# Optimization experiments

Hardware: AMD Instinct MI355X
Metric: run time of the kernel (lower is better)

## Reference

```python
import jax, jax.numpy as jnp
import numpy as np


def setup_inputs() -> dict:
    key = jax.random.key(0)
    k1, k2 = jax.random.split(key)
    B, N, M = 32, 4096, 4096
    pred = jax.random.normal(k1, (B, N, 3), dtype=jnp.float32)
    target = jax.random.normal(k2, (B, M, 3), dtype=jnp.float32)
    return {"pred": pred, "target": target}


def reference(pred, target):
    # pairwise euclidean distances: [B, N, M]
    # d2 = |p|^2 + |t|^2 - 2 p.t  (matches torch.cdist p=2)
    p2 = jnp.sum(pred * pred, axis=-1)                      # [B, N]
    t2 = jnp.sum(target * target, axis=-1)                  # [B, M]
    pt = jnp.einsum('bnd,bmd->bnm', pred, target)           # [B, N, M]
    d2 = p2[:, :, None] + t2[:, None, :] - 2.0 * pt
    dist = jnp.sqrt(jnp.maximum(d2, 0.0))                   # [B, N, M]
    min_d = jnp.min(dist, axis=2)                           # [B, N]
    return jnp.mean(min_d)
```

## Files before the change

kernel.cpp:

```cpp
#include <hip/hip_runtime.h>


typedef short bf16x8 __attribute__((ext_vector_type(8)));
typedef float f32x16 __attribute__((ext_vector_type(16)));

constexpr int Bc = 32;
constexpr int Nc = 4096;
constexpr int Mc = 4096;
constexpr int BLOCK = 512;
constexpr int PTS = Bc * Nc;
constexpr int S = 4;
constexpr int TPB = 1024;
constexpr int PPB = 512;
constexpr unsigned POISON = 0xAAAAAAAAu;

__device__ __forceinline__ unsigned short brne(float x) {
  unsigned u = __float_as_uint(x);
  return (unsigned short)((u + 0x7FFFu + ((u >> 16) & 1u)) >> 16);
}
__device__ __forceinline__ float bf2f(unsigned short h) {
  return __uint_as_float(((unsigned)h) << 16);
}
__device__ __forceinline__ unsigned pack(unsigned short lo, unsigned short hi) {
  return (unsigned)lo | ((unsigned)hi << 16);
}

__global__ __launch_bounds__(BLOCK)
__attribute__((amdgpu_waves_per_eu(8, 8)))
void emd_fused_kernel(const float* __restrict__ pred,
                      const float* __restrict__ target,
                      unsigned* __restrict__ minb,
                      unsigned* __restrict__ cnts,
                      float* __restrict__ out) {
  __shared__ uint4 lds[2048];

  const int pg = blockIdx.x >> 2;
  const int s = blockIdx.x & 3;
  const int b = pg >> 3;
  const int lane = threadIdx.x & 63;
  const int half = lane >> 5;
  const int l31 = lane & 31;
  const int wave = threadIdx.x >> 6;
  const int tid = threadIdx.x;
  const unsigned short ONE = 0x3F80;

  float px, py, pz;
  {
    const size_t gi = (size_t)pg * PPB + tid;
    px = pred[3 * gi]; py = pred[3 * gi + 1]; pz = pred[3 * gi + 2];
  }
  const size_t tbase = (size_t)b * Mc + s * TPB;
  float tx[2], ty[2], tz[2];
#pragma unroll
  for (int j = 0; j < 2; ++j) {
    const size_t ti = tbase + tid + j * 512;
    tx[j] = target[3 * ti]; ty[j] = target[3 * ti + 1];
    tz[j] = target[3 * ti + 2];
  }

  uint4 t0[2];
#pragma unroll
  for (int j = 0; j < 2; ++j) {
    float X = -2.0f * tx[j], Y = -2.0f * ty[j], Z = -2.0f * tz[j];
    unsigned short Xh = brne(X), Xl = brne(X - bf2f(Xh));
    unsigned short Yh = brne(Y), Yl = brne(Y - bf2f(Yh));
    unsigned short Zh = brne(Z), Zl = brne(Z - bf2f(Zh));
    float t2 = 0.25f * fmaf(X, X, fmaf(Y, Y, Z * Z));
    unsigned short th = brne(t2), tl = brne(t2 - bf2f(th));
    t0[j] = make_uint4(pack(Xh, Xh), pack(Xl, Yh), pack(Yh, Yl), pack(Zh, Zh));
    lds[1024 + tid + j * 512] =
        make_uint4(pack(Zl, th), pack(tl, ONE), pack(ONE, 0), 0);
  }

  {
    float x = px, y = py, z = pz;
    unsigned short xh = brne(x), xl = brne(x - bf2f(xh));
    unsigned short yh = brne(y), yl = brne(y - bf2f(yh));
    unsigned short zh = brne(z), zl = brne(z - bf2f(zh));
    float p2 = fmaf(x, x, fmaf(y, y, z * z));
    unsigned short ph = brne(p2), pl = brne(p2 - bf2f(ph));
    lds[tid] =
        make_uint4(pack(xh, xl), pack(xh, yh), pack(yl, yh), pack(zh, zl));
    lds[512 + tid] = make_uint4(pack(zh, ONE), pack(ONE, ph), pack(pl, 0), 0);
  }
  __syncthreads();

  bf16x8 bfr[2];
#pragma unroll
  for (int f = 0; f < 2; ++f) {
    uint4 u = lds[half * 512 + wave * 64 + f * 32 + l31];
    bfr[f] = *(const bf16x8*)&u;
  }
  __syncthreads();

#pragma unroll
  for (int j = 0; j < 2; ++j) lds[tid + j * 512] = t0[j];
  __syncthreads();

  float rA[2], rB[2];
#pragma unroll
  for (int f = 0; f < 2; ++f) { rA[f] = 3.4e38f; rB[f] = 3.4e38f; }

  const int abase = half * 1024 + l31;
#pragma unroll 2
  for (int t = 0; t < 32; ++t) {
    uint4 au = lds[abase + t * 32];
    bf16x8 af = *(const bf16x8*)&au;
    f32x16 z{};
    f32x16 d0 = __builtin_amdgcn_mfma_f32_32x32x16_bf16(af, bfr[0], z, 0, 0, 0);
    f32x16 d1 = __builtin_amdgcn_mfma_f32_32x32x16_bf16(af, bfr[1], z, 0, 0, 0);
#pragma unroll
    for (int i = 0; i < 16; i += 4) {
      rA[0] = fminf(fminf(d0[i], d0[i + 1]), rA[0]);
      rB[0] = fminf(fminf(d0[i + 2], d0[i + 3]), rB[0]);
      rA[1] = fminf(fminf(d1[i], d1[i + 1]), rA[1]);
      rB[1] = fminf(fminf(d1[i + 2], d1[i + 3]), rB[1]);
    }
  }

  const unsigned gbase = (unsigned)pg * PPB + wave * 64;
#pragma unroll
  for (int f = 0; f < 2; ++f) {
    float rr = fminf(rA[f], rB[f]);
    rr = fminf(rr, __shfl_xor(rr, 32, 64));
    if (lane < 32)
      __hip_atomic_fetch_min(&minb[gbase + f * 32 + l31],
                             __float_as_uint(fmaxf(rr, 0.0f)),
                             __ATOMIC_RELAXED, __HIP_MEMORY_SCOPE_AGENT);
  }

  asm volatile("s_waitcnt vmcnt(0)" ::: "memory");
  __syncthreads();

  unsigned* lflag = (unsigned*)lds;
  if (tid == 0) {
    unsigned old = __hip_atomic_fetch_add(&cnts[pg], 1u, __ATOMIC_RELAXED,
                                          __HIP_MEMORY_SCOPE_AGENT);
    lflag[0] = (old == POISON + (S - 1) || old == (unsigned)(S - 1)) ? 1u : 0u;
  }
  __syncthreads();
  if (lflag[0]) {
    const unsigned base = (unsigned)pg * PPB;
    unsigned ub = __hip_atomic_load(&minb[base + tid], __ATOMIC_RELAXED,
                                    __HIP_MEMORY_SCOPE_AGENT);
    float ssum = sqrtf(__uint_as_float(ub));
#pragma unroll
    for (int off = 32; off > 0; off >>= 1) ssum += __shfl_down(ssum, off, 64);
    float* lsum = (float*)lds;
    if (lane == 0) lsum[1 + wave] = ssum;
    __syncthreads();
    if (tid == 0) {
      float tot = 0.0f;
#pragma unroll
      for (int w = 0; w < 8; ++w) tot += lsum[1 + w];
      atomicAdd(out, tot * (1.0f / (float)PTS));
    }
  }
}

extern "C" void kernel_launch(void* const* d_in, const int* in_sizes, int n_in,
                              void* d_out, int out_size, void* d_ws, size_t ws_size,
                              hipStream_t stream) {
  const float* pred = (const float*)d_in[0];
  const float* target = (const float*)d_in[1];
  unsigned* minb = (unsigned*)d_ws;
  unsigned* cnts = minb + PTS;
  emd_fused_kernel<<<dim3((PTS / PPB) * S), dim3(BLOCK), 0, stream>>>(
      pred, target, minb, cnts, (float*)d_out);
}
```

Measured before the change: 72.92 us.

## Loop over target splits in-block with double-buffered LDS instead of atomic cross-block min

```diff
diff --git a/kernel.cpp b/kernel.cpp
--- a/kernel.cpp
+++ b/kernel.cpp
@@ -10,9 +10,8 @@
 constexpr int BLOCK = 512;
 constexpr int PTS = Bc * Nc;
 constexpr int S = 4;
-constexpr int TPB = 1024;
-constexpr int PPB = 512;
-constexpr unsigned POISON = 0xAAAAAAAAu;
+constexpr int TPS = 1024;
+constexpr int PPB = 256;
 
 __device__ __forceinline__ unsigned short brne(float x) {
   unsigned u = __float_as_uint(x);
@@ -24,19 +23,17 @@
 __device__ __forceinline__ unsigned pack(unsigned short lo, unsigned short hi) {
   return (unsigned)lo | ((unsigned)hi << 16);
 }
+__device__ __forceinline__ int imin(int a, int b) { return a < b ? a : b; }
 
 __global__ __launch_bounds__(BLOCK)
-__attribute__((amdgpu_waves_per_eu(8, 8)))
+__attribute__((amdgpu_waves_per_eu(4, 4)))
 void emd_fused_kernel(const float* __restrict__ pred,
                       const float* __restrict__ target,
-                      unsigned* __restrict__ minb,
-                      unsigned* __restrict__ cnts,
                       float* __restrict__ out) {
-  __shared__ uint4 lds[2048];
+  __shared__ uint4 lds[4608];
 
-  const int pg = blockIdx.x >> 2;
-  const int s = blockIdx.x & 3;
-  const int b = pg >> 3;
+  const int pg = blockIdx.x;
+  const int b = pg >> 4;
   const int lane = threadIdx.x & 63;
   const int half = lane >> 5;
   const int l31 = lane & 31;
@@ -44,21 +41,20 @@
   const int tid = threadIdx.x;
   const unsigned short ONE = 0x3F80;
 
-  float px, py, pz;
-  {
+  float px = 0.f, py = 0.f, pz = 0.f;
+  if (tid < PPB) {
     const size_t gi = (size_t)pg * PPB + tid;
     px = pred[3 * gi]; py = pred[3 * gi + 1]; pz = pred[3 * gi + 2];
   }
-  const size_t tbase = (size_t)b * Mc + s * TPB;
+  const size_t tb = (size_t)b * Mc;
   float tx[2], ty[2], tz[2];
 #pragma unroll
   for (int j = 0; j < 2; ++j) {
-    const size_t ti = tbase + tid + j * 512;
+    const size_t ti = tb + tid + j * 512;
     tx[j] = target[3 * ti]; ty[j] = target[3 * ti + 1];
     tz[j] = target[3 * ti + 2];
   }
 
-  uint4 t0[2];
 #pragma unroll
   for (int j = 0; j < 2; ++j) {
     float X = -2.0f * tx[j], Y = -2.0f * ty[j], Z = -2.0f * tz[j];
@@ -67,94 +63,94 @@
     unsigned short Zh = brne(Z), Zl = brne(Z - bf2f(Zh));
     float t2 = 0.25f * fmaf(X, X, fmaf(Y, Y, Z * Z));
     unsigned short th = brne(t2), tl = brne(t2 - bf2f(th));
-    t0[j] = make_uint4(pack(Xh, Xh), pack(Xl, Yh), pack(Yh, Yl), pack(Zh, Zh));
-    lds[1024 + tid + j * 512] =
+    lds[512 + tid + j * 512] =
+        make_uint4(pack(Xh, Xh), pack(Xl, Yh), pack(Yh, Yl), pack(Zh, Zh));
+    lds[512 + 1024 + tid + j * 512] =
         make_uint4(pack(Zl, th), pack(tl, ONE), pack(ONE, 0), 0);
   }
 
-  {
-    float x = px, y = py, z = pz;
-    unsigned short xh = brne(x), xl = brne(x - bf2f(xh));
-    unsigned short yh = brne(y), yl = brne(y - bf2f(yh));
-    unsigned short zh = brne(z), zl = brne(z - bf2f(zh));
-    float p2 = fmaf(x, x, fmaf(y, y, z * z));
+  if (tid < PPB) {
+    unsigned short xh = brne(px), xl = brne(px - bf2f(xh));
+    unsigned short yh = brne(py), yl = brne(py - bf2f(yh));
+    unsigned short zh = brne(pz), zl = brne(pz - bf2f(zh));
+    float p2 = fmaf(px, px, fmaf(py, py, pz * pz));
     unsigned short ph = brne(p2), pl = brne(p2 - bf2f(ph));
     lds[tid] =
         make_uint4(pack(xh, xl), pack(xh, yh), pack(yl, yh), pack(zh, zl));
-    lds[512 + tid] = make_uint4(pack(zh, ONE), pack(ONE, ph), pack(pl, 0), 0);
+    lds[PPB + tid] = make_uint4(pack(zh, ONE), pack(ONE, ph), pack(pl, 0), 0);
   }
   __syncthreads();
 
-  bf16x8 bfr[2];
+  bf16x8 bfr;
+  {
+    uint4 u = lds[half * PPB + wave * 32 + l31];
+    bfr = *(const bf16x8*)&u;
+  }
+
+  int rA = 0x7F7FFFFF, rB = 0x7F7FFFFF;
+#pragma unroll 1
+  for (int s = 0; s < S; ++s) {
+    if (s < 3) {
 #pragma unroll
-  for (int f = 0; f < 2; ++f) {
-    uint4 u = lds[half * 512 + wave * 64 + f * 32 + l31];
-    bfr[f] = *(const bf16x8*)&u;
-  }
-  __syncthreads();
-
+      for (int j = 0; j < 2; ++j) {
+        const size_t ti = tb + (s + 1) * TPS + tid + j * 512;
+        tx[j] = target[3 * ti]; ty[j] = target[3 * ti + 1];
+        tz[j] = target[3 * ti + 2];
+      }
+    }
+    const int abase = 512 + (s & 1) * 2048 + half * 1024 + l31;
+#pragma unroll 2
+    for (int t = 0; t < 32; ++t) {
+      uint4 au = lds[abase + t * 32];
+      bf16x8 af = *(const bf16x8*)&au;
+      f32x16 z{};
+      f32x16 d =
+          __builtin_amdgcn_mfma_f32_32x32x16_bf16(af, bfr, z, 0, 0, 0);
 #pragma unroll
-  for (int j = 0; j < 2; ++j) lds[tid + j * 512] = t0[j];
-  __syncthreads();
-
-  float rA[2], rB[2];
+      for (int i = 0; i < 16; i += 4) {
+        rA = imin(imin(__float_as_int(d[i]), __float_as_int(d[i + 1])), rA);
+        rB = imin(imin(__float_as_int(d[i + 2]), __float_as_int(d[i + 3])),
+                  rB);
+      }
+    }
+    if (s < 3) {
+      __syncthreads();
 #pragma unroll
-  for (int f = 0; f < 2; ++f) { rA[f] = 3.4e38f; rB[f] = 3.4e38f; }
-
-  const int abase = half * 1024 + l31;
-#pragma unroll 2
-  for (int t = 0; t < 32; ++t) {
-    uint4 au = lds[abase + t * 32];
-    bf16x8 af = *(const bf16x8*)&au;
-    f32x16 z{};
-    f32x16 d0 = __builtin_amdgcn_mfma_f32_32x32x16_bf16(af, bfr[0], z, 0, 0, 0);
-    f32x16 d1 = __builtin_amdgcn_mfma_f32_32x32x16_bf16(af, bfr[1], z, 0, 0, 0);
-#pragma unroll
-    for (int i = 0; i < 16; i += 4) {
-      rA[0] = fminf(fminf(d0[i], d0[i + 1]), rA[0]);
-      rB[0] = fminf(fminf(d0[i + 2], d0[i + 3]), rB[0]);
-      rA[1] = fminf(fminf(d1[i], d1[i + 1]), rA[1]);
-      rB[1] = fminf(fminf(d1[i + 2], d1[i + 3]), rB[1]);
+      for (int j = 0; j < 2; ++j) {
+        float X = -2.0f * tx[j], Y = -2.0f * ty[j], Z = -2.0f * tz[j];
+        unsigned short Xh = brne(X), Xl = brne(X - bf2f(Xh));
+        unsigned short Yh = brne(Y), Yl = brne(Y - bf2f(Yh));
+        unsigned short Zh = brne(Z), Zl = brne(Z - bf2f(Zh));
+        float t2 = 0.25f * fmaf(X, X, fmaf(Y, Y, Z * Z));
+        unsigned short th = brne(t2), tl = brne(t2 - bf2f(th));
+        const int base = 512 + ((s + 1) & 1) * 2048 + tid + j * 512;
+        lds[base] =
+            make_uint4(pack(Xh, Xh), pack(Xl, Yh), pack(Yh, Yl), pack(Zh, Zh));
+        lds[base + 1024] =
+            make_uint4(pack(Zl, th), pack(tl, ONE), pack(ONE, 0), 0);
+      }
+      __syncthreads();
     }
   }
 
-  const unsigned gbase = (unsigned)pg * PPB + wave * 64;
-#pragma unroll
-  for (int f = 0; f < 2; ++f) {
-    float rr = fminf(rA[f], rB[f]);
-    rr = fminf(rr, __shfl_xor(rr, 32, 64));
-    if (lane < 32)
-      __hip_atomic_fetch_min(&minb[gbase + f * 32 + l31],
-                             __float_as_uint(fmaxf(rr, 0.0f)),
-                             __ATOMIC_RELAXED, __HIP_MEMORY_SCOPE_AGENT);
-  }
-
-  asm volatile("s_waitcnt vmcnt(0)" ::: "memory");
-  __syncthreads();
-
-  unsigned* lflag = (unsigned*)lds;
-  if (tid == 0) {
-    unsigned old = __hip_atomic_fetch_add(&cnts[pg], 1u, __ATOMIC_RELAXED,
-                                          __HIP_MEMORY_SCOPE_AGENT);
-    lflag[0] = (old == POISON + (S - 1) || old == (unsigned)(S - 1)) ? 1u : 0u;
+  float* fm = (float*)lds;
+  {
+    int rr = imin(rA, rB);
+    rr = imin(rr, __shfl_xor(rr, 32, 64));
+    rr = rr < 0 ? 0 : rr;
+    if (lane < 32) fm[wave * 32 + l31] = sqrtf(__uint_as_float((unsigned)rr));
   }
   __syncthreads();
-  if (lflag[0]) {
-    const unsigned base = (unsigned)pg * PPB;
-    unsigned ub = __hip_atomic_load(&minb[base + tid], __ATOMIC_RELAXED,
-                                    __HIP_MEMORY_SCOPE_AGENT);
-    float ssum = sqrtf(__uint_as_float(ub));
+  if (tid < PPB) {
+    float v = fm[tid];
 #pragma unroll
-    for (int off = 32; off > 0; off >>= 1) ssum += __shfl_down(ssum, off, 64);
-    float* lsum = (float*)lds;
-    if (lane == 0) lsum[1 + wave] = ssum;
-    __syncthreads();
-    if (tid == 0) {
-      float tot = 0.0f;
-#pragma unroll
-      for (int w = 0; w < 8; ++w) tot += lsum[1 + w];
-      atomicAdd(out, tot * (1.0f / (float)PTS));
-    }
+    for (int off = 32; off > 0; off >>= 1) v += __shfl_down(v, off, 64);
+    if (lane == 0) fm[256 + (tid >> 6)] = v;
+  }
+  __syncthreads();
+  if (tid == 0) {
+    float tot = (fm[256] + fm[257]) + (fm[258] + fm[259]);
+    atomicAdd(out, tot * (1.0f / (float)PTS));
   }
 }
 
@@ -163,8 +159,7 @@
                               hipStream_t stream) {
   const float* pred = (const float*)d_in[0];
   const float* target = (const float*)d_in[1];
-  unsigned* minb = (unsigned*)d_ws;
-  unsigned* cnts = minb + PTS;
-  emd_fused_kernel<<<dim3((PTS / PPB) * S), dim3(BLOCK), 0, stream>>>(
-      pred, target, minb, cnts, (float*)d_out);
+  (void)d_ws; (void)ws_size;
+  emd_fused_kernel<<<dim3(PTS / PPB), dim3(BLOCK), 0, stream>>>(
+      pred, target, (float*)d_out);
 }
```

Result: slower. 76.56 us (+5.0%).
